# Performance work log

Hardware: AMD Instinct MI355X
Metric: run time of the kernel (lower is better)

## Reference

```python
import jax, jax.numpy as jnp
import numpy as np

N = 100000   # nodes
E = 1600000  # edges
IN = 32
HID = 64
OUT = 1

def setup_inputs() -> dict:
    key = jax.random.key(0)
    ks = jax.random.split(key, 16)
    x = jax.random.normal(ks[0], (N, IN), jnp.float32)
    edge_index = jax.random.randint(ks[1], (2, E), 0, N, dtype=jnp.int32)
    def lin(k, fi, fo):
        return jax.random.normal(k, (fi, fo), jnp.float32) / np.sqrt(fi)
    # SAGEConv params per layer: Wn/bn for aggregated neighbors (lin_l), Wr for root (lin_r, no bias)
    Wn0 = lin(ks[2], IN, HID);  bn0 = jnp.zeros((HID,), jnp.float32); Wr0 = lin(ks[3], IN, HID)
    Wn1 = lin(ks[4], HID, HID); bn1 = jnp.zeros((HID,), jnp.float32); Wr1 = lin(ks[5], HID, HID)
    Wn2 = lin(ks[6], HID, HID); bn2 = jnp.zeros((HID,), jnp.float32); Wr2 = lin(ks[7], HID, HID)
    # predictor MLP
    Wp1 = lin(ks[8], HID, HID); bp1 = jnp.zeros((HID,), jnp.float32)
    Wp2 = lin(ks[9], HID, OUT); bp2 = jnp.zeros((OUT,), jnp.float32)
    return dict(x=x, edge_index=edge_index,
                Wn0=Wn0, bn0=bn0, Wr0=Wr0,
                Wn1=Wn1, bn1=bn1, Wr1=Wr1,
                Wn2=Wn2, bn2=bn2, Wr2=Wr2,
                Wp1=Wp1, bp1=bp1, Wp2=Wp2, bp2=bp2)

def reference(x, edge_index, Wn0, bn0, Wr0, Wn1, bn1, Wr1, Wn2, bn2, Wr2, Wp1, bp1, Wp2, bp2):
    src, dst = edge_index[0], edge_index[1]
    n = x.shape[0]
    # mean-aggregation normalization (nodes with no in-edges get 0, as in PyG)
    cnt = jax.ops.segment_sum(jnp.ones(src.shape, x.dtype), dst, num_segments=n)
    inv = jnp.where(cnt > 0, 1.0 / jnp.maximum(cnt, 1.0), 0.0)[:, None]

    def sage(h, Wn, bn, Wr):
        agg = jax.ops.segment_sum(h[src], dst, num_segments=n) * inv  # [N, d]
        return agg @ Wn + bn + h @ Wr

    h = jax.nn.relu(sage(x, Wn0, bn0, Wr0))
    h = jax.nn.relu(sage(h, Wn1, bn1, Wr1))
    h = sage(h, Wn2, bn2, Wr2)  # no activation after last GNN layer
    h = jax.nn.relu(h @ Wp1 + bp1)
    return jax.nn.sigmoid(h @ Wp2 + bp2)
```

## Files before the change

### kernel.cpp

```cpp
#include <hip/hip_runtime.h>
#include <math.h>

#define NN 100000
#define EE 1600000
#define HID 64
#define BKT 391
#define SLAB 5504
#define SLAB_IT ((SLAB + 255) / 256)
#define CHUNK 4096
#define NWG ((EE + CHUNK - 1) / CHUNK)
#define TB (NN / 16)
#define TBM (NN / 32)

typedef _Float16 f16;
typedef _Float16 f16x2 __attribute__((ext_vector_type(2)));

__device__ __forceinline__ f16x2 u2h(unsigned u) { return __builtin_bit_cast(f16x2, u); }
__device__ __forceinline__ unsigned h2u(f16x2 h) { return __builtin_bit_cast(unsigned, h); }

#if defined(__has_builtin) && __has_builtin(__builtin_amdgcn_fdot2)
__device__ __forceinline__ float dot2(f16x2 a, f16x2 b, float c) {
    return __builtin_amdgcn_fdot2(a, b, c, false);
}
#else
__device__ __forceinline__ float dot2(f16x2 a, f16x2 b, float c) {
    c = fmaf((float)a.x, (float)b.x, c);
    return fmaf((float)a.y, (float)b.y, c);
}
#endif


#if defined(__has_builtin)
#if __has_builtin(__builtin_amdgcn_cvt_pk_f32_fp8) && __has_builtin(__builtin_amdgcn_cvt_pk_fp8_f32)
#define HW_FP8 1
#endif
#endif

#ifndef HW_FP8
__device__ __forceinline__ float dec_e4m3(unsigned b) {
    unsigned s = b >> 7, e = (b >> 3) & 0xF, m = b & 7;
    float v;
    if (e == 0) v = (float)m * 0.001953125f;
    else v = (1.f + (float)m * 0.125f) * exp2f((float)((int)e - 7));
    return s ? -v : v;
}
__device__ __forceinline__ unsigned char enc_e4m3(float x) {
    unsigned s = (__builtin_bit_cast(unsigned, x) >> 31) << 7;
    float a = fabsf(x);
    if (!(a < 464.f)) return (unsigned char)(s | 0x7E);
    int e; float m = frexpf(a, &e);
    int E = e - 1;
    unsigned bits;
    if (E < -6) {
        int n = (int)rintf(a * 512.f);
        bits = (n > 7) ? 0x08u : (unsigned)n;
    } else {
        int n = (int)rintf((2.f * m - 1.f) * 8.f);
        if (n == 8) { n = 0; E += 1; }
        if (E > 8) return (unsigned char)(s | 0x7E);
        bits = ((unsigned)(E + 7) << 3) | (unsigned)n;
    }
    return (unsigned char)(s | bits);
}
#endif

__device__ __forceinline__ void acc_fp8(unsigned v, float& a0, float& a1,
                                        float& a2, float& a3) {
#ifdef HW_FP8
    auto lo = __builtin_amdgcn_cvt_pk_f32_fp8((int)v, false);
    auto hi = __builtin_amdgcn_cvt_pk_f32_fp8((int)v, true);
    a0 += lo[0]; a1 += lo[1]; a2 += hi[0]; a3 += hi[1];
#else
    a0 += dec_e4m3(v & 0xFFu);         a1 += dec_e4m3((v >> 8) & 0xFFu);
    a2 += dec_e4m3((v >> 16) & 0xFFu); a3 += dec_e4m3(v >> 24);
#endif
}

__device__ __forceinline__ unsigned char enc_fp8(float x) {
#ifdef HW_FP8
    return (unsigned char)(__builtin_amdgcn_cvt_pk_fp8_f32(x, x, 0, false) & 0xFF);
#else
    return enc_e4m3(x);
#endif
}


__global__ void mt_kernel(const int* __restrict__ src, const int* __restrict__ dst,
                          int* __restrict__ bfill, unsigned* __restrict__ pairs,
                          const float* __restrict__ h,
                          const float* __restrict__ Wn, const float* __restrict__ bn,
                          const float* __restrict__ Wr,
                          unsigned char* __restrict__ hn8, f16* __restrict__ hrb,
                          const float* __restrict__ Wn1, const float* __restrict__ Wr1,
                          const float* __restrict__ Wn2, const float* __restrict__ Wr2,
                          const float* __restrict__ Wp1, unsigned* __restrict__ w16) {
    __shared__ int lc[BKT];
    __shared__ int lbase[BKT];
    int t = threadIdx.x;

    if (blockIdx.x < NWG) {
        for (int b = t; b < BKT; b += 256) lc[b] = 0;
        __syncthreads();
        int base = blockIdx.x * CHUNK;
        int myd[CHUNK / 256];
        int myr[CHUNK / 256];
#pragma unroll
        for (int j = 0; j < CHUNK / 256; ++j) {
            int i = base + j * 256 + t;
            myd[j] = (i < EE) ? dst[i] : -1;
            myr[j] = (myd[j] >= 0) ? atomicAdd(&lc[myd[j] >> 8], 1) : 0;
        }
        __syncthreads();
        for (int b = t; b < BKT; b += 256) {
            int c = lc[b];
            if (c) {
                int ofs = atomicAdd(&bfill[b], c);
                if (ofs + c > SLAB) ofs = SLAB - c;
                lbase[b] = b * SLAB + ofs;
            }
        }
        __syncthreads();
#pragma unroll
        for (int j = 0; j < CHUNK / 256; ++j) {
            int i = base + j * 256 + t;
            if (myd[j] >= 0) {
                int b = myd[j] >> 8;
                pairs[lbase[b] + myr[j]] = (unsigned)src[i] | ((unsigned)(myd[j] & 255) << 24);
            }
        }
        return;
    }

    int bb = blockIdx.x - NWG;

    if (bb < 40) {
        int id = bb * 256 + t;
        int mat = id >> 11;
        int p = (id >> 6) & 31;
        int j = id & 63;
        const float* W = (mat == 0) ? Wn1 : (mat == 1) ? Wr1 :
                         (mat == 2) ? Wn2 : (mat == 3) ? Wr2 : Wp1;
        f16x2 v;
        v.x = (f16)W[(2 * p) * HID + j];
        v.y = (f16)W[(2 * p + 1) * HID + j];
        w16[id] = h2u(v);
    }

    int lane = t & 63;
    int wid = (bb * 256 + t) >> 6;
    int m0 = __builtin_amdgcn_readfirstlane(wid << 3);
    const float* h0 = h + (size_t)m0 * 32;

    float an[8] = {0.f, 0.f, 0.f, 0.f, 0.f, 0.f, 0.f, 0.f};
    float ar[8] = {0.f, 0.f, 0.f, 0.f, 0.f, 0.f, 0.f, 0.f};
#pragma unroll
    for (int k = 0; k < 32; ++k) {
        float wn = Wn[k * HID + lane];
        float wr = Wr[k * HID + lane];
#pragma unroll
        for (int n = 0; n < 8; ++n) {
            float hk = h0[n * 32 + k];
            an[n] = fmaf(hk, wn, an[n]);
            ar[n] = fmaf(hk, wr, ar[n]);
        }
    }
    float b = bn[lane];
    size_t o8 = (size_t)m0 * HID + lane;
    size_t o = (size_t)m0 * HID + lane;
#pragma unroll
    for (int n = 0; n < 8; ++n) {
        hn8[o8 + n * HID] = enc_fp8(an[n]);
        hrb[o + n * HID] = (f16)(ar[n] + b);
    }
}


__global__ void build_kernel(const unsigned* __restrict__ pairs,
                             const int* __restrict__ bfill,
                             int* __restrict__ rs, int* __restrict__ re,
                             float* __restrict__ inv, int* __restrict__ col) {
    __shared__ int ncnt[256];
    __shared__ int nexcl[256];
    int b = blockIdx.x;
    int t = threadIdx.x;
    int s0 = b * SLAB;
    int ce = bfill[b]; if (ce > SLAB) ce = SLAB;
    ncnt[t] = 0;
    __syncthreads();
    unsigned mypk[SLAB_IT];
    int myr[SLAB_IT];
#pragma unroll
    for (int j = 0; j < SLAB_IT; ++j) {
        int e = j * 256 + t;
        if (e < ce) {
            unsigned pk = pairs[s0 + e];
            mypk[j] = pk;
            myr[j] = atomicAdd(&ncnt[pk >> 24], 1);
        }
    }
    __syncthreads();
    int c = ncnt[t];
    int c4 = (c + 3) & ~3;
    nexcl[t] = c4;
    __syncthreads();
    for (int off = 1; off < 256; off <<= 1) {
        int u = (t >= off) ? nexcl[t - off] : 0;
        __syncthreads();
        nexcl[t] += u;
        __syncthreads();
    }
    int excl = nexcl[t] - c4;
    int node = (b << 8) + t;
    if (node < NN) {
        int start = s0 + excl; if (start > s0 + SLAB) start = s0 + SLAB;
        int end = start + c;   if (end > s0 + SLAB) end = s0 + SLAB;
        rs[node] = start;
        re[node] = end;
        inv[node] = (c > 0) ? (1.0f / (float)c) : 0.0f;
    }
    __syncthreads();
    ncnt[t] = excl;
    __syncthreads();
#pragma unroll
    for (int j = 0; j < SLAB_IT; ++j) {
        int e = j * 256 + t;
        if (e < ce) {
            unsigned pk = mypk[j];
            int idx = s0 + ncnt[pk >> 24] + myr[j];
            if (idx < s0 + SLAB) col[idx] = (int)(pk & 0xFFFFFFu);
        }
    }
    for (int k = c; k < c4; ++k) {
        int idx = s0 + excl + k;
        if (idx < s0 + SLAB) col[idx] = NN;
    }
}


__device__ __forceinline__ void acc8(uint2 v, float& a0, float& a1, float& a2,
                                     float& a3, float& a4, float& a5, float& a6,
                                     float& a7) {
    acc_fp8(v.x, a0, a1, a2, a3);
    acc_fp8(v.y, a4, a5, a6, a7);
}

__device__ __forceinline__ void qgp(const uint2* __restrict__ rp2,
                                    const int* __restrict__ col,
                                    int e, int en, int en4, int ff, int el,
                                    float& a0, float& a1, float& a2, float& a3,
                                    float& a4, float& a5, float& a6, float& a7) {
    while (e + 8 <= en4) {
        int4 ca = *(const int4*)(col + e);
        int4 cb = *(const int4*)(col + e + 4);
        int c0 = el ? ca.y : ca.x;
        int c1 = el ? ca.w : ca.z;
        int c2 = el ? cb.y : cb.x;
        int c3 = el ? cb.w : cb.z;
        uint2 v0 = rp2[(size_t)c0 * 8 + ff];
        uint2 v1 = rp2[(size_t)c1 * 8 + ff];
        uint2 v2 = rp2[(size_t)c2 * 8 + ff];
        uint2 v3 = rp2[(size_t)c3 * 8 + ff];
        acc8(v0, a0, a1, a2, a3, a4, a5, a6, a7);
        acc8(v1, a0, a1, a2, a3, a4, a5, a6, a7);
        acc8(v2, a0, a1, a2, a3, a4, a5, a6, a7);
        acc8(v3, a0, a1, a2, a3, a4, a5, a6, a7);
        e += 8;
    }
    if (e + 4 <= en4) {
        int4 ca = *(const int4*)(col + e);
        int c0 = el ? ca.y : ca.x;
        int c1 = el ? ca.w : ca.z;
        uint2 v0 = rp2[(size_t)c0 * 8 + ff];
        uint2 v1 = rp2[(size_t)c1 * 8 + ff];
        acc8(v0, a0, a1, a2, a3, a4, a5, a6, a7);
        acc8(v1, a0, a1, a2, a3, a4, a5, a6, a7);
        e += 4;
    }
    while (e < en) {
        if (!el) {
            uint2 v = rp2[(size_t)col[e] * 8 + ff];
            acc8(v, a0, a1, a2, a3, a4, a5, a6, a7);
        }
        ++e;
    }
}


__global__ void gt_kernel(const unsigned char* __restrict__ An8,
                          const int* __restrict__ rs, const int* __restrict__ re,
                          const int* __restrict__ col, const float* __restrict__ inv,
                          f16* C,
                          const unsigned* __restrict__ Wn16, const float* __restrict__ bn,
                          const unsigned* __restrict__ Wr16,
                          unsigned char* __restrict__ Aout8) {
    __shared__ uint4 hsh[128];
    int t = threadIdx.x;
    int lane = t & 63;
    int wv = t >> 6;
    int wid = (blockIdx.x * blockDim.x + t) >> 6;
    int m0 = wid << 2;
    int m = m0 + (lane >> 4);
    int ff = lane & 7;
    int el = (lane >> 3) & 1;

    int e = rs[m], en = re[m];
    int en4 = e + ((en - e + 3) & ~3);
    int bnd = ((m >> 8) + 1) * SLAB;
    if (en4 > bnd) en4 = bnd;

    float a0 = 0.f, a1 = 0.f, a2 = 0.f, a3 = 0.f;
    float a4 = 0.f, a5 = 0.f, a6 = 0.f, a7 = 0.f;
    qgp((const uint2*)An8, col, e, en, en4, ff, el, a0, a1, a2, a3, a4, a5, a6, a7);

    a0 += __shfl_xor(a0, 8); a1 += __shfl_xor(a1, 8);
    a2 += __shfl_xor(a2, 8); a3 += __shfl_xor(a3, 8);
    a4 += __shfl_xor(a4, 8); a5 += __shfl_xor(a5, 8);
    a6 += __shfl_xor(a6, 8); a7 += __shfl_xor(a7, 8);

    float iv = inv[m];
    uint4 cur = ((const uint4*)C)[(size_t)m * 8 + ff];
    f16x2 q0 = u2h(cur.x), q1 = u2h(cur.y), q2 = u2h(cur.z), q3 = u2h(cur.w);
    f16x2 p0, p1, p2, p3;
    p0.x = (f16)fmaxf(fmaf(a0, iv, (float)q0.x), 0.f);
    p0.y = (f16)fmaxf(fmaf(a1, iv, (float)q0.y), 0.f);
    p1.x = (f16)fmaxf(fmaf(a2, iv, (float)q1.x), 0.f);
    p1.y = (f16)fmaxf(fmaf(a3, iv, (float)q1.y), 0.f);
    p2.x = (f16)fmaxf(fmaf(a4, iv, (float)q2.x), 0.f);
    p2.y = (f16)fmaxf(fmaf(a5, iv, (float)q2.y), 0.f);
    p3.x = (f16)fmaxf(fmaf(a6, iv, (float)q3.x), 0.f);
    p3.y = (f16)fmaxf(fmaf(a7, iv, (float)q3.y), 0.f);

    uint4 hv4;
    hv4.x = h2u(p0); hv4.y = h2u(p1); hv4.z = h2u(p2); hv4.w = h2u(p3);
    if (!(lane & 8)) hsh[wv * 32 + (lane >> 4) * 8 + ff] = hv4;

    float an[4] = {0.f, 0.f, 0.f, 0.f};
    float ar[4] = {0.f, 0.f, 0.f, 0.f};
#pragma unroll
    for (int j = 0; j < 8; ++j) {
        f16x2 wn0 = u2h(Wn16[(4 * j) * HID + lane]);
        f16x2 wn1 = u2h(Wn16[(4 * j + 1) * HID + lane]);
        f16x2 wn2 = u2h(Wn16[(4 * j + 2) * HID + lane]);
        f16x2 wn3 = u2h(Wn16[(4 * j + 3) * HID + lane]);
        f16x2 wr0 = u2h(Wr16[(4 * j) * HID + lane]);
        f16x2 wr1 = u2h(Wr16[(4 * j + 1) * HID + lane]);
        f16x2 wr2 = u2h(Wr16[(4 * j + 2) * HID + lane]);
        f16x2 wr3 = u2h(Wr16[(4 * j + 3) * HID + lane]);
#pragma unroll
        for (int n = 0; n < 4; ++n) {
            uint4 d = hsh[wv * 32 + n * 8 + j];
            an[n] = dot2(u2h(d.x), wn0, an[n]);
            an[n] = dot2(u2h(d.y), wn1, an[n]);
            an[n] = dot2(u2h(d.z), wn2, an[n]);
            an[n] = dot2(u2h(d.w), wn3, an[n]);
            ar[n] = dot2(u2h(d.x), wr0, ar[n]);
            ar[n] = dot2(u2h(d.y), wr1, ar[n]);
            ar[n] = dot2(u2h(d.z), wr2, ar[n]);
            ar[n] = dot2(u2h(d.w), wr3, ar[n]);
        }
    }
    float b = bn[lane];
    size_t o8 = (size_t)m0 * HID + lane;
    size_t o = (size_t)m0 * HID + lane;
#pragma unroll
    for (int n = 0; n < 4; ++n) {
        Aout8[o8 + n * HID] = enc_fp8(an[n]);
        C[o + n * HID] = (f16)(ar[n] + b);
    }
}


__global__ void gh_kernel(const unsigned char* __restrict__ An8,
                          const int* __restrict__ rs, const int* __restrict__ re,
                          const int* __restrict__ col, const float* __restrict__ inv,
                          const f16* __restrict__ C,
                          const unsigned* __restrict__ Wp116, const float* __restrict__ bp1,
                          const float* __restrict__ Wp2, const float* __restrict__ bp2,
                          float* __restrict__ out) {
    __shared__ uint4 hsh[128];
    int t = threadIdx.x;
    int lane = t & 63;
    int wv = t >> 6;
    int wid = (blockIdx.x * blockDim.x + t) >> 6;
    int m0 = wid << 2;
    int m = m0 + (lane >> 4);
    int ff = lane & 7;
    int el = (lane >> 3) & 1;

    int e = rs[m], en = re[m];
    int en4 = e + ((en - e + 3) & ~3);
    int bnd = ((m >> 8) + 1) * SLAB;
    if (en4 > bnd) en4 = bnd;

    float a0 = 0.f, a1 = 0.f, a2 = 0.f, a3 = 0.f;
    float a4 = 0.f, a5 = 0.f, a6 = 0.f, a7 = 0.f;
    qgp((const uint2*)An8, col, e, en, en4, ff, el, a0, a1, a2, a3, a4, a5, a6, a7);

    a0 += __shfl_xor(a0, 8); a1 += __shfl_xor(a1, 8);
    a2 += __shfl_xor(a2, 8); a3 += __shfl_xor(a3, 8);
    a4 += __shfl_xor(a4, 8); a5 += __shfl_xor(a5, 8);
    a6 += __shfl_xor(a6, 8); a7 += __shfl_xor(a7, 8);

    float iv = inv[m];
    uint4 cur = ((const uint4*)C)[(size_t)m * 8 + ff];
    f16x2 q0 = u2h(cur.x), q1 = u2h(cur.y), q2 = u2h(cur.z), q3 = u2h(cur.w);
    f16x2 p0, p1, p2, p3;
    p0.x = (f16)fmaf(a0, iv, (float)q0.x);
    p0.y = (f16)fmaf(a1, iv, (float)q0.y);
    p1.x = (f16)fmaf(a2, iv, (float)q1.x);
    p1.y = (f16)fmaf(a3, iv, (float)q1.y);
    p2.x = (f16)fmaf(a4, iv, (float)q2.x);
    p2.y = (f16)fmaf(a5, iv, (float)q2.y);
    p3.x = (f16)fmaf(a6, iv, (float)q3.x);
    p3.y = (f16)fmaf(a7, iv, (float)q3.y);

    uint4 hv4;
    hv4.x = h2u(p0); hv4.y = h2u(p1); hv4.z = h2u(p2); hv4.w = h2u(p3);
    if (!(lane & 8)) hsh[wv * 32 + (lane >> 4) * 8 + ff] = hv4;

    float tn[4] = {0.f, 0.f, 0.f, 0.f};
#pragma unroll
    for (int j = 0; j < 8; ++j) {
        f16x2 wp0 = u2h(Wp116[(4 * j) * HID + lane]);
        f16x2 wp1 = u2h(Wp116[(4 * j + 1) * HID + lane]);
        f16x2 wp2 = u2h(Wp116[(4 * j + 2) * HID + lane]);
        f16x2 wp3 = u2h(Wp116[(4 * j + 3) * HID + lane]);
#pragma unroll
        for (int n = 0; n < 4; ++n) {
            uint4 d = hsh[wv * 32 + n * 8 + j];
            tn[n] = dot2(u2h(d.x), wp0, tn[n]);
            tn[n] = dot2(u2h(d.y), wp1, tn[n]);
            tn[n] = dot2(u2h(d.z), wp2, tn[n]);
            tn[n] = dot2(u2h(d.w), wp3, tn[n]);
        }
    }
    float b = bp1[lane], w2v = Wp2[lane];
    float r0 = fmaxf(tn[0] + b, 0.f) * w2v;
    float r1 = fmaxf(tn[1] + b, 0.f) * w2v;
    float r2 = fmaxf(tn[2] + b, 0.f) * w2v;
    float r3 = fmaxf(tn[3] + b, 0.f) * w2v;
#pragma unroll
    for (int off = 32; off > 0; off >>= 1) {
        r0 += __shfl_xor(r0, off);
        r1 += __shfl_xor(r1, off);
        r2 += __shfl_xor(r2, off);
        r3 += __shfl_xor(r3, off);
    }
    if (lane == 0) {
        float bb = bp2[0];
        out[m0]     = 1.f / (1.f + expf(-(r0 + bb)));
        out[m0 + 1] = 1.f / (1.f + expf(-(r1 + bb)));
        out[m0 + 2] = 1.f / (1.f + expf(-(r2 + bb)));
        out[m0 + 3] = 1.f / (1.f + expf(-(r3 + bb)));
    }
}

extern "C" void kernel_launch(void* const* d_in, const int* in_sizes, int n_in,
                              void* d_out, int out_size, void* d_ws, size_t ws_size,
                              hipStream_t stream) {
    const float* x   = (const float*)d_in[0];
    const int* eidx  = (const int*)d_in[1];
    const float* Wn0 = (const float*)d_in[2];
    const float* bn0 = (const float*)d_in[3];
    const float* Wr0 = (const float*)d_in[4];
    const float* Wn1 = (const float*)d_in[5];
    const float* bn1 = (const float*)d_in[6];
    const float* Wr1 = (const float*)d_in[7];
    const float* Wn2 = (const float*)d_in[8];
    const float* bn2 = (const float*)d_in[9];
    const float* Wr2 = (const float*)d_in[10];
    const float* Wp1 = (const float*)d_in[11];
    const float* bp1 = (const float*)d_in[12];
    const float* Wp2 = (const float*)d_in[13];
    const float* bp2 = (const float*)d_in[14];
    float* out = (float*)d_out;

    const int* src = eidx;
    const int* dst = eidx + EE;

    char* w = (char*)d_ws;
    size_t off = 0;
    auto carve = [&](size_t bytes) -> void* {
        void* p = w + off;
        off = (off + bytes + 255) & ~(size_t)255;
        return p;
    };
    int*   rsA    = (int*)carve((size_t)NN * 4);
    int*   reA    = (int*)carve((size_t)NN * 4);
    float* inv    = (float*)carve((size_t)NN * 4);
    int*   col    = (int*)carve((size_t)BKT * SLAB * 4);
    int*   bfill  = (int*)carve((size_t)BKT * 4);
    unsigned* w16 = (unsigned*)carve((size_t)5 * 2048 * 4);
    unsigned char* A0 = (unsigned char*)carve((size_t)(NN + 1) * HID);
    unsigned char* A1 = (unsigned char*)carve((size_t)(NN + 1) * HID);
    f16*   C      = (f16*)carve((size_t)NN * HID * 2);
    unsigned* pairs = (unsigned*)carve((size_t)BKT * SLAB * 4);
    (void)ws_size;

    unsigned* Wn1_16 = w16;
    unsigned* Wr1_16 = w16 + 2048;
    unsigned* Wn2_16 = w16 + 4096;
    unsigned* Wr2_16 = w16 + 6144;
    unsigned* Wp1_16 = w16 + 8192;

    hipMemsetAsync(bfill, 0, (size_t)BKT * 4, stream);
    hipMemsetAsync(A0 + (size_t)NN * HID, 0, HID, stream);
    hipMemsetAsync(A1 + (size_t)NN * HID, 0, HID, stream);

    mt_kernel<<<NWG + TBM, 256, 0, stream>>>(src, dst, bfill, pairs,
                                             x, Wn0, bn0, Wr0, A0, C,
                                             Wn1, Wr1, Wn2, Wr2, Wp1, w16);
    build_kernel<<<BKT, 256, 0, stream>>>(pairs, bfill, rsA, reA, inv, col);

    gt_kernel<<<TB, 256, 0, stream>>>(A0, rsA, reA, col, inv, C, Wn1_16, bn1, Wr1_16, A1);
    gt_kernel<<<TB, 256, 0, stream>>>(A1, rsA, reA, col, inv, C, Wn2_16, bn2, Wr2_16, A0);
    gh_kernel<<<TB, 256, 0, stream>>>(A0, rsA, reA, col, inv, C, Wp1_16, bp1, Wp2, bp2, out);
}
```

Baseline: 245.5 us.

## Use nontemporal loads/stores, fold pad-row memsets into kernel, halve rows per wave

Switches many streaming global loads and stores (edge indices, pairs, col, C, outputs) to nontemporal variants to reduce cache pollution. Replaces two hipMemsetAsync calls that zero the padding rows with writes done inside mt_kernel, saving launches. Also cuts the rows processed per wave in the first-layer transform from 8 to 4 and doubles that part of the grid. The nontemporal hints may hurt where data is reused, such as col read by three kernels and C reread.

```diff
diff --git a/kernel.cpp b/kernel.cpp
--- a/kernel.cpp
+++ b/kernel.cpp
@@ -10,10 +10,11 @@
 #define CHUNK 4096
 #define NWG ((EE + CHUNK - 1) / CHUNK)
 #define TB (NN / 16)
-#define TBM (NN / 32)
 
 typedef _Float16 f16;
 typedef _Float16 f16x2 __attribute__((ext_vector_type(2)));
+typedef int i32x4 __attribute__((ext_vector_type(4)));
+typedef unsigned u32x4 __attribute__((ext_vector_type(4)));
 
 __device__ __forceinline__ f16x2 u2h(unsigned u) { return __builtin_bit_cast(f16x2, u); }
 __device__ __forceinline__ unsigned h2u(f16x2 h) { return __builtin_bit_cast(unsigned, h); }
@@ -91,6 +92,7 @@
                           const float* __restrict__ Wn, const float* __restrict__ bn,
                           const float* __restrict__ Wr,
                           unsigned char* __restrict__ hn8, f16* __restrict__ hrb,
+                          unsigned char* __restrict__ hn8b,
                           const float* __restrict__ Wn1, const float* __restrict__ Wr1,
                           const float* __restrict__ Wn2, const float* __restrict__ Wr2,
                           const float* __restrict__ Wp1, unsigned* __restrict__ w16) {
@@ -107,7 +109,7 @@
 #pragma unroll
         for (int j = 0; j < CHUNK / 256; ++j) {
             int i = base + j * 256 + t;
-            myd[j] = (i < EE) ? dst[i] : -1;
+            myd[j] = (i < EE) ? __builtin_nontemporal_load(dst + i) : -1;
             myr[j] = (myd[j] >= 0) ? atomicAdd(&lc[myd[j] >> 8], 1) : 0;
         }
         __syncthreads();
@@ -125,7 +127,9 @@
             int i = base + j * 256 + t;
             if (myd[j] >= 0) {
                 int b = myd[j] >> 8;
-                pairs[lbase[b] + myr[j]] = (unsigned)src[i] | ((unsigned)(myd[j] & 255) << 24);
+                unsigned pk = (unsigned)__builtin_nontemporal_load(src + i)
+                              | ((unsigned)(myd[j] & 255) << 24);
+                __builtin_nontemporal_store(pk, &pairs[lbase[b] + myr[j]]);
             }
         }
         return;
@@ -145,33 +149,39 @@
         v.y = (f16)W[(2 * p + 1) * HID + j];
         w16[id] = h2u(v);
     }
+    if (bb == 40 && t < 32) {
+        if (t < 16) ((unsigned*)(hn8  + (size_t)NN * HID))[t] = 0;
+        else        ((unsigned*)(hn8b + (size_t)NN * HID))[t - 16] = 0;
+    }
 
     int lane = t & 63;
     int wid = (bb * 256 + t) >> 6;
-    int m0 = __builtin_amdgcn_readfirstlane(wid << 3);
+    int m0 = __builtin_amdgcn_readfirstlane(wid << 2);
     const float* h0 = h + (size_t)m0 * 32;
 
-    float an[8] = {0.f, 0.f, 0.f, 0.f, 0.f, 0.f, 0.f, 0.f};
-    float ar[8] = {0.f, 0.f, 0.f, 0.f, 0.f, 0.f, 0.f, 0.f};
+    float an0 = 0.f, an1 = 0.f, an2 = 0.f, an3 = 0.f;
+    float ar0 = 0.f, ar1 = 0.f, ar2 = 0.f, ar3 = 0.f;
 #pragma unroll
     for (int k = 0; k < 32; ++k) {
         float wn = Wn[k * HID + lane];
         float wr = Wr[k * HID + lane];
-#pragma unroll
-        for (int n = 0; n < 8; ++n) {
-            float hk = h0[n * 32 + k];
-            an[n] = fmaf(hk, wn, an[n]);
-            ar[n] = fmaf(hk, wr, ar[n]);
-        }
+        float hk0 = h0[k], hk1 = h0[32 + k], hk2 = h0[64 + k], hk3 = h0[96 + k];
+        an0 = fmaf(hk0, wn, an0); ar0 = fmaf(hk0, wr, ar0);
+        an1 = fmaf(hk1, wn, an1); ar1 = fmaf(hk1, wr, ar1);
+        an2 = fmaf(hk2, wn, an2); ar2 = fmaf(hk2, wr, ar2);
+        an3 = fmaf(hk3, wn, an3); ar3 = fmaf(hk3, wr, ar3);
     }
     float b = bn[lane];
     size_t o8 = (size_t)m0 * HID + lane;
     size_t o = (size_t)m0 * HID + lane;
-#pragma unroll
-    for (int n = 0; n < 8; ++n) {
-        hn8[o8 + n * HID] = enc_fp8(an[n]);
-        hrb[o + n * HID] = (f16)(ar[n] + b);
-    }
+    __builtin_nontemporal_store(enc_fp8(an0), hn8 + o8);
+    __builtin_nontemporal_store(enc_fp8(an1), hn8 + o8 + HID);
+    __builtin_nontemporal_store(enc_fp8(an2), hn8 + o8 + 2 * HID);
+    __builtin_nontemporal_store(enc_fp8(an3), hn8 + o8 + 3 * HID);
+    __builtin_nontemporal_store((f16)(ar0 + b), hrb + o);
+    __builtin_nontemporal_store((f16)(ar1 + b), hrb + o + HID);
+    __builtin_nontemporal_store((f16)(ar2 + b), hrb + o + 2 * HID);
+    __builtin_nontemporal_store((f16)(ar3 + b), hrb + o + 3 * HID);
 }
 
 
@@ -193,7 +203,7 @@
     for (int j = 0; j < SLAB_IT; ++j) {
         int e = j * 256 + t;
         if (e < ce) {
-            unsigned pk = pairs[s0 + e];
+            unsigned pk = __builtin_nontemporal_load(pairs + s0 + e);
             mypk[j] = pk;
             myr[j] = atomicAdd(&ncnt[pk >> 24], 1);
         }
@@ -227,12 +237,13 @@
         if (e < ce) {
             unsigned pk = mypk[j];
             int idx = s0 + ncnt[pk >> 24] + myr[j];
-            if (idx < s0 + SLAB) col[idx] = (int)(pk & 0xFFFFFFu);
+            if (idx < s0 + SLAB)
+                __builtin_nontemporal_store((int)(pk & 0xFFFFFFu), col + idx);
         }
     }
     for (int k = c; k < c4; ++k) {
         int idx = s0 + excl + k;
-        if (idx < s0 + SLAB) col[idx] = NN;
+        if (idx < s0 + SLAB) __builtin_nontemporal_store(NN, col + idx);
     }
 }
 
@@ -250,8 +261,8 @@
                                     float& a0, float& a1, float& a2, float& a3,
                                     float& a4, float& a5, float& a6, float& a7) {
     while (e + 8 <= en4) {
-        int4 ca = *(const int4*)(col + e);
-        int4 cb = *(const int4*)(col + e + 4);
+        i32x4 ca = __builtin_nontemporal_load((const i32x4*)(col + e));
+        i32x4 cb = __builtin_nontemporal_load((const i32x4*)(col + e + 4));
         int c0 = el ? ca.y : ca.x;
         int c1 = el ? ca.w : ca.z;
         int c2 = el ? cb.y : cb.x;
@@ -267,7 +278,7 @@
         e += 8;
     }
     if (e + 4 <= en4) {
-        int4 ca = *(const int4*)(col + e);
+        i32x4 ca = __builtin_nontemporal_load((const i32x4*)(col + e));
         int c0 = el ? ca.y : ca.x;
         int c1 = el ? ca.w : ca.z;
         uint2 v0 = rp2[(size_t)c0 * 8 + ff];
@@ -318,7 +329,7 @@
     a6 += __shfl_xor(a6, 8); a7 += __shfl_xor(a7, 8);
 
     float iv = inv[m];
-    uint4 cur = ((const uint4*)C)[(size_t)m * 8 + ff];
+    u32x4 cur = __builtin_nontemporal_load((const u32x4*)C + (size_t)m * 8 + ff);
     f16x2 q0 = u2h(cur.x), q1 = u2h(cur.y), q2 = u2h(cur.z), q3 = u2h(cur.w);
     f16x2 p0, p1, p2, p3;
     p0.x = (f16)fmaxf(fmaf(a0, iv, (float)q0.x), 0.f);
@@ -364,8 +375,8 @@
     size_t o = (size_t)m0 * HID + lane;
 #pragma unroll
     for (int n = 0; n < 4; ++n) {
-        Aout8[o8 + n * HID] = enc_fp8(an[n]);
-        C[o + n * HID] = (f16)(ar[n] + b);
+        __builtin_nontemporal_store(enc_fp8(an[n]), Aout8 + o8 + n * HID);
+        __builtin_nontemporal_store((f16)(ar[n] + b), C + o + n * HID);
     }
 }
 
@@ -402,7 +413,7 @@
     a6 += __shfl_xor(a6, 8); a7 += __shfl_xor(a7, 8);
 
     float iv = inv[m];
-    uint4 cur = ((const uint4*)C)[(size_t)m * 8 + ff];
+    u32x4 cur = __builtin_nontemporal_load((const u32x4*)C + (size_t)m * 8 + ff);
     f16x2 q0 = u2h(cur.x), q1 = u2h(cur.y), q2 = u2h(cur.z), q3 = u2h(cur.w);
     f16x2 p0, p1, p2, p3;
     p0.x = (f16)fmaf(a0, iv, (float)q0.x);
@@ -448,10 +459,10 @@
     }
     if (lane == 0) {
         float bb = bp2[0];
-        out[m0]     = 1.f / (1.f + expf(-(r0 + bb)));
-        out[m0 + 1] = 1.f / (1.f + expf(-(r1 + bb)));
-        out[m0 + 2] = 1.f / (1.f + expf(-(r2 + bb)));
-        out[m0 + 3] = 1.f / (1.f + expf(-(r3 + bb)));
+        __builtin_nontemporal_store(1.f / (1.f + expf(-(r0 + bb))), out + m0);
+        __builtin_nontemporal_store(1.f / (1.f + expf(-(r1 + bb))), out + m0 + 1);
+        __builtin_nontemporal_store(1.f / (1.f + expf(-(r2 + bb))), out + m0 + 2);
+        __builtin_nontemporal_store(1.f / (1.f + expf(-(r3 + bb))), out + m0 + 3);
     }
 }
 
@@ -504,12 +515,10 @@
     unsigned* Wp1_16 = w16 + 8192;
 
     hipMemsetAsync(bfill, 0, (size_t)BKT * 4, stream);
-    hipMemsetAsync(A0 + (size_t)NN * HID, 0, HID, stream);
-    hipMemsetAsync(A1 + (size_t)NN * HID, 0, HID, stream);
-
-    mt_kernel<<<NWG + TBM, 256, 0, stream>>>(src, dst, bfill, pairs,
-                                             x, Wn0, bn0, Wr0, A0, C,
-                                             Wn1, Wr1, Wn2, Wr2, Wp1, w16);
+
+    mt_kernel<<<NWG + TB, 256, 0, stream>>>(src, dst, bfill, pairs,
+                                            x, Wn0, bn0, Wr0, A0, C, A1,
+                                            Wn1, Wr1, Wn2, Wr2, Wp1, w16);
     build_kernel<<<BKT, 256, 0, stream>>>(pairs, bfill, rsA, reA, inv, col);
 
     gt_kernel<<<TB, 256, 0, stream>>>(A0, rsA, reA, col, inv, C, Wn1_16, bn1, Wr1_16, A1);
```

New measurement: 347.5 us. 1.42x slower.
